# Optimization experiments

Measured on AMD Instinct MI355X. Metric: run time of the kernel, lower is better.

## Reference

```python
import jax, jax.numpy as jnp
import numpy as np

LAMBDA_SOFTMAX = 10.0  # opt.lambda_softmax
LEAKY_SLOPE = 0.1


def l2norm(x, axis):
    # matches torch F.normalize(p=2, eps=1e-12)
    n = jnp.linalg.norm(x, axis=axis, keepdims=True)
    return x / jnp.clip(n, 1e-12)


def setup_inputs() -> dict:
    key = jax.random.key(0)
    k1, k2, k3, k4, k5 = jax.random.split(key, 5)
    I, Q, T, S, D = 64, 49, 64, 64, 256  # n_img, n_region, n_txt, max_words, feature_size
    return {
        "local_img_query": jax.random.normal(k1, (I, Q, D), jnp.float32),
        "local_img_value": jax.random.normal(k2, (I, Q, D), jnp.float32),
        "local_text_key": jax.random.normal(k3, (T, S, D), jnp.float32),
        "local_text_value": jax.random.normal(k4, (T, S, D), jnp.float32),
        "text_length": jax.random.randint(k5, (T,), 8, S + 1, jnp.int32),
    }


def reference(local_img_query, local_img_value, local_text_key, local_text_value, text_length):
    # Vectorized form of the per-sentence Python loop in compute_i2t_sim.
    # Variable sentence lengths are handled with a mask over the padded word axis,
    # which reproduces the ragged torch math exactly (see comments).
    T, S, D = local_text_key.shape
    I, Q, _ = local_img_query.shape

    qn = l2norm(local_img_query, -1)   # [I,Q,D]
    kn = l2norm(local_text_key, -1)    # [T,S,D]

    # bmm(txt_key_norm, queryT): (B,S,D)x(B,D,Q) -> here [T,I,S,Q]
    attn = jnp.einsum('tsd,iqd->tisq', kn, qn)
    attn = jnp.where(attn > 0, attn, LEAKY_SLOPE * attn)      # LeakyReLU(0.1)
    # l2norm(attn, 2) normalizes over queryL per (t,i,s) row -> independent of padding
    attn = l2norm(attn, -1)
    attn = jnp.swapaxes(attn, 2, 3)                            # [T,I,Q,S]

    mask = jnp.arange(S)[None, :] < text_length[:, None]       # [T,S]
    logits = jnp.where(mask[:, None, None, :], attn * LAMBDA_SOFTMAX, -jnp.inf)
    attn = jax.nn.softmax(logits, axis=-1)                     # padded words -> exactly 0

    # focal_equal with sourceL = actual n_word of each sentence
    n_word = text_length.astype(attn.dtype)[:, None, None, None]
    funcF = attn * n_word - jnp.sum(attn, axis=-1, keepdims=True)
    fattn = (funcF > 0).astype(attn.dtype)                     # padded attn=0 -> funcF<0 -> 0
    tmp = fattn * attn
    attn = tmp / jnp.sum(tmp, axis=-1, keepdims=True)

    # bmm(valueT, attnT) -> weighted text context per (txt, img): [T,I,Q,D]
    wei = jnp.einsum('tsd,tiqs->tiqd', local_text_value, attn)
    wei = l2norm(wei, -1)

    # cosine similarity with image values along d, then mean over regions
    v = local_img_value[None]                                  # [1,I,Q,D]
    w12 = jnp.sum(v * wei, -1)
    denom = jnp.linalg.norm(v, axis=-1) * jnp.linalg.norm(wei, axis=-1)
    sim = w12 / jnp.clip(denom, 1e-8)                          # [T,I,Q]
    i2t = sim.mean(axis=-1)                                    # [T,I]
    return i2t.T                                               # [n_img, n_txt]
```

## Files before the change

### kernel.cpp

```cpp
#include <hip/hip_runtime.h>
#include <math.h>

#define I_N 64
#define Q_N 49
#define T_N 64
#define S_N 64
#define D_N 256

typedef __attribute__((ext_vector_type(8))) short short8;
typedef __attribute__((ext_vector_type(4))) float f32x4;
typedef unsigned short ushort_t;

__device__ __forceinline__ float waveReduceSum64(float v) {
    v += __shfl_xor(v, 1);
    v += __shfl_xor(v, 2);
    v += __shfl_xor(v, 4);
    v += __shfl_xor(v, 8);
    v += __shfl_xor(v, 16);
    v += __shfl_xor(v, 32);
    return v;
}

__device__ __forceinline__ ushort_t f2bf(float x) {
    unsigned u = __builtin_bit_cast(unsigned, x);
    unsigned r = (u + 0x7fffu + ((u >> 16) & 1u)) >> 16;
    return (ushort_t)r;
}
__device__ __forceinline__ float bf2f(ushort_t h) {
    unsigned u = ((unsigned)h) << 16;
    return __builtin_bit_cast(float, u);
}
__device__ __forceinline__ void split_bf16(float x, ushort_t& h, ushort_t& l) {
    h = f2bf(x);
    l = f2bf(x - bf2f(h));
}

__global__ void prep_all(const float* __restrict__ q_in, const float* __restrict__ v_in,
                         const float* __restrict__ k_in, const float* __restrict__ tv,
                         ushort_t* __restrict__ qfh, ushort_t* __restrict__ qfl,
                         ushort_t* __restrict__ kfh, ushort_t* __restrict__ kfl,
                         ushort_t* __restrict__ vfh, ushort_t* __restrict__ vfl,
                         float* __restrict__ vP, float* __restrict__ vnorm) {
    __shared__ float tile[64][65];
    __shared__ float ws[8];
    int b = blockIdx.x;
    int tid = threadIdx.x;

    if (b < 8192) {
        int isimg = (b < 4096) ? 1 : 0;
        int row = isimg ? b : (b - 4096);
        int hi = row >> 6, lo = row & 63;
        float x = 0.0f, vv = 0.0f;
        if (isimg) {
            if (lo < Q_N) {
                size_t base = ((size_t)hi * Q_N + lo) * D_N + tid;
                x = q_in[base];
                vv = v_in[base];
            }
        } else {
            x = k_in[(size_t)row * D_N + tid];
        }
        float s1 = waveReduceSum64(x * x);
        float s2 = waveReduceSum64(vv * vv);
        int wv = tid >> 6, ln = tid & 63;
        if (ln == 0) { ws[wv] = s1; ws[4 + wv] = s2; }
        __syncthreads();
        float n1 = sqrtf(ws[0] + ws[1] + ws[2] + ws[3]);
        float xn = x / fmaxf(n1, 1e-12f);
        ushort_t h, l;
        split_bf16(xn, h, l);
        size_t off = ((size_t)hi << 14) + (size_t)((((lo >> 4) * 8 + (tid >> 5))) << 9)
                   + (size_t)(((((tid >> 3) & 3) * 16 + (lo & 15))) << 3) + (tid & 7);
        if (isimg) {
            qfh[off] = h;
            qfl[off] = l;
            if (tid == 0) vnorm[row] = sqrtf(ws[4] + ws[5] + ws[6] + ws[7]);
        } else {
            kfh[off] = h;
            kfl[off] = l;
        }
    } else if (b < 8448) {
        int bb = b - 8192;
        int t = bb >> 2;
        int d0 = (bb & 3) * 64;
        const float* src = tv + ((size_t)t << 14) + d0;
        ushort_t* dh = vfh + ((size_t)t << 14);
        ushort_t* dl = vfl + ((size_t)t << 14);
#pragma unroll
        for (int r = 0; r < 16; ++r) {
            int idx = r * 256 + tid;
            int s = idx >> 6, d = idx & 63;
            tile[s][d] = src[s * D_N + d];
        }
        __syncthreads();
#pragma unroll
        for (int r = 0; r < 16; ++r) {
            int idx = r * 256 + tid;
            int d = idx >> 6, s = idx & 63;
            int dg = d0 + d;
            float x = tile[s][d];
            ushort_t h, l;
            split_bf16(x, h, l);
            int dgrp = dg >> 4, lrd = dg & 15;
            int k0g = s >> 5, lk3 = (s >> 3) & 3, e = s & 7;
            size_t off = (size_t)(dgrp << 10) + (k0g << 9) + ((lk3 * 16 + lrd) << 3) + e;
            dh[off] = h;
            dl[off] = l;
        }
    } else {
        int bb = b - 8448;
        int i = bb >> 3;
        int sub = bb & 7;
        const float* src = v_in + (size_t)i * Q_N * D_N;
        float* dst = vP + ((size_t)i << 14);
#pragma unroll
        for (int r2 = 0; r2 < 8; ++r2) {
            int rep = sub * 8 + r2;
            int o = rep * 256 + tid;
            int r = o & 3;
            int md = (o >> 2) & 3;
            int nq = (o >> 4) & 3;
            int lane = (o >> 6) & 63;
            int w = o >> 12;
            int lr = lane & 15, lk = lane >> 4;
            int q = nq * 16 + lr;
            int d = w * 64 + md * 16 + lk * 4 + r;
            dst[o] = (q < Q_N) ? src[q * D_N + d] : 0.0f;
        }
    }
}

__launch_bounds__(256, 4)
__global__ void i2t_mfma(const ushort_t* __restrict__ kfh, const ushort_t* __restrict__ kfl,
                         const ushort_t* __restrict__ qfh, const ushort_t* __restrict__ qfl,
                         const ushort_t* __restrict__ vfh, const ushort_t* __restrict__ vfl,
                         const float* __restrict__ vP,
                         const float* __restrict__ vnorm,
                         const int* __restrict__ tlen,
                         float* __restrict__ out)
{
    __shared__ __align__(16) unsigned char RK[33280];

    const int bid = blockIdx.x;
    const int xcd = bid & 7;
    const int j = bid >> 3;
    const int t = (xcd << 3) | (j & 7);
    const int i = j >> 3;

    const int tid = threadIdx.x;
    const int lane = tid & 63;
    const int w = tid >> 6;
    const int lr = lane & 15;
    const int lk = lane >> 4;

    const int wsr = (w >> 1) * 32;
    const int wq  = (w & 1) * 32;
    f32x4 acc[2][2];
#pragma unroll
    for (int a = 0; a < 2; ++a)
#pragma unroll
        for (int b2 = 0; b2 < 2; ++b2) acc[a][b2] = (f32x4){0.f, 0.f, 0.f, 0.f};
    {
        const ushort_t* kH = kfh + ((size_t)t << 14) + (size_t)(w >> 1) * 8192;
        const ushort_t* kL = kfl + ((size_t)t << 14) + (size_t)(w >> 1) * 8192;
        const ushort_t* qH = qfh + ((size_t)i << 14) + (size_t)(w & 1) * 8192;
        const ushort_t* qL = qfl + ((size_t)i << 14) + (size_t)(w & 1) * 8192;
#pragma unroll
        for (int k8 = 0; k8 < 8; ++k8) {
            int fo = k8 * 512 + lane * 8;
            short8 aH0 = *(const short8*)(kH + fo);
            short8 aL0 = *(const short8*)(kL + fo);
            short8 aH1 = *(const short8*)(kH + 4096 + fo);
            short8 aL1 = *(const short8*)(kL + 4096 + fo);
            short8 bH0 = *(const short8*)(qH + fo);
            short8 bL0 = *(const short8*)(qL + fo);
            short8 bH1 = *(const short8*)(qH + 4096 + fo);
            short8 bL1 = *(const short8*)(qL + 4096 + fo);
            acc[0][0] = __builtin_amdgcn_mfma_f32_16x16x32_bf16(aH0, bH0, acc[0][0], 0, 0, 0);
            acc[0][1] = __builtin_amdgcn_mfma_f32_16x16x32_bf16(aH0, bH1, acc[0][1], 0, 0, 0);
            acc[1][0] = __builtin_amdgcn_mfma_f32_16x16x32_bf16(aH1, bH0, acc[1][0], 0, 0, 0);
            acc[1][1] = __builtin_amdgcn_mfma_f32_16x16x32_bf16(aH1, bH1, acc[1][1], 0, 0, 0);
            acc[0][0] = __builtin_amdgcn_mfma_f32_16x16x32_bf16(aH0, bL0, acc[0][0], 0, 0, 0);
            acc[0][1] = __builtin_amdgcn_mfma_f32_16x16x32_bf16(aH0, bL1, acc[0][1], 0, 0, 0);
            acc[1][0] = __builtin_amdgcn_mfma_f32_16x16x32_bf16(aH1, bL0, acc[1][0], 0, 0, 0);
            acc[1][1] = __builtin_amdgcn_mfma_f32_16x16x32_bf16(aH1, bL1, acc[1][1], 0, 0, 0);
            acc[0][0] = __builtin_amdgcn_mfma_f32_16x16x32_bf16(aL0, bH0, acc[0][0], 0, 0, 0);
            acc[0][1] = __builtin_amdgcn_mfma_f32_16x16x32_bf16(aL0, bH1, acc[0][1], 0, 0, 0);
            acc[1][0] = __builtin_amdgcn_mfma_f32_16x16x32_bf16(aL1, bH0, acc[1][0], 0, 0, 0);
            acc[1][1] = __builtin_amdgcn_mfma_f32_16x16x32_bf16(aL1, bH1, acc[1][1], 0, 0, 0);
        }
    }
    {
        float* As = (float*)RK;
#pragma unroll
        for (int si = 0; si < 2; ++si)
#pragma unroll
            for (int qi = 0; qi < 2; ++qi)
#pragma unroll
                for (int r = 0; r < 4; ++r) {
                    int s = wsr + si * 16 + lk * 4 + r;
                    int q = wq + qi * 16 + lr;
                    float v = acc[si][qi][r];
                    v = (v > 0.0f) ? v : 0.1f * v;
                    As[s * 65 + q] = v;
                }
    }
    __syncthreads();

    {
        const float* As = (const float*)RK;
        float* rinv = (float*)(RK + 16640);
        int s = tid >> 2, part = tid & 3;
        float ss = 0.0f;
#pragma unroll
        for (int q0 = 0; q0 < 64; q0 += 4) {
            float v = As[s * 65 + q0 + part];
            ss += v * v;
        }
        ss += __shfl_xor(ss, 1);
        ss += __shfl_xor(ss, 2);
        if (part == 0) rinv[s] = 1.0f / fmaxf(sqrtf(ss), 1e-12f);
    }
    __syncthreads();

    const int len = tlen[t];
    {
        const float* As = (const float*)RK;
        const float* rinv = (const float*)(RK + 16640);
        ushort_t* Ph = (ushort_t*)(RK + 16896);
        ushort_t* Pl = (ushort_t*)(RK + 25088);
        const float thr = 1.0f / (float)len;
        int q = tid >> 2, part = tid & 3;
        float logit[16];
        float m = -INFINITY;
#pragma unroll
        for (int k = 0; k < 16; ++k) {
            int s = part * 16 + k;
            float lg = (s < len) ? 10.0f * As[s * 65 + q] * rinv[s] : -INFINITY;
            logit[k] = lg;
            m = fmaxf(m, lg);
        }
        m = fmaxf(m, __shfl_xor(m, 1));
        m = fmaxf(m, __shfl_xor(m, 2));
        float p[16];
        float sum = 0.0f;
#pragma unroll
        for (int k = 0; k < 16; ++k) {
            int s = part * 16 + k;
            float e = (s < len) ? __expf(logit[k] - m) : 0.0f;
            p[k] = e;
            sum += e;
        }
        sum += __shfl_xor(sum, 1);
        sum += __shfl_xor(sum, 2);
        float inv = 1.0f / sum;
        float sk = 0.0f;
#pragma unroll
        for (int k = 0; k < 16; ++k) {
            p[k] *= inv;
            if (p[k] > thr) sk += p[k];
        }
        sk += __shfl_xor(sk, 1);
        sk += __shfl_xor(sk, 2);
        float iv2 = 1.0f / sk;

        ushort_t hh[16], ll[16];
#pragma unroll
        for (int k = 0; k < 16; ++k) {
            float pv = (p[k] > thr) ? p[k] * iv2 : 0.0f;
            if (q >= Q_N) pv = 0.0f;
            split_bf16(pv, hh[k], ll[k]);
        }
        int c0 = (2 * part) ^ (q & 7);
        int c1 = (2 * part + 1) ^ (q & 7);
        short8 v0, v1;
#pragma unroll
        for (int k = 0; k < 8; ++k) { v0[k] = (short)hh[k]; v1[k] = (short)hh[k + 8]; }
        *(short8*)(Ph + q * 64 + (c0 << 3)) = v0;
        *(short8*)(Ph + q * 64 + (c1 << 3)) = v1;
#pragma unroll
        for (int k = 0; k < 8; ++k) { v0[k] = (short)ll[k]; v1[k] = (short)ll[k + 8]; }
        *(short8*)(Pl + q * 64 + (c0 << 3)) = v0;
        *(short8*)(Pl + q * 64 + (c1 << 3)) = v1;
    }
    __syncthreads();

    f32x4 acc2[4][4];
#pragma unroll
    for (int a = 0; a < 4; ++a)
#pragma unroll
        for (int b2 = 0; b2 < 4; ++b2) acc2[a][b2] = (f32x4){0.f, 0.f, 0.f, 0.f};
    {
        const ushort_t* vH = vfh + ((size_t)t << 14) + (size_t)w * 4096;
        const ushort_t* vL = vfl + ((size_t)t << 14) + (size_t)w * 4096;
        const ushort_t* PH = (const ushort_t*)(RK + 16896);
        const ushort_t* PL = (const ushort_t*)(RK + 25088);
#pragma unroll
        for (int k0g = 0; k0g < 2; ++k0g) {
#pragma unroll
            for (int md = 0; md < 4; ++md) {
                int vo = md * 1024 + k0g * 512 + lane * 8;
                short8 vh = *(const short8*)(vH + vo);
                short8 vl = *(const short8*)(vL + vo);
#pragma unroll
                for (int nq = 0; nq < 4; ++nq) {
                    int qrow = nq * 16 + lr;
                    int o = qrow * 64 + (((k0g * 4 + lk) ^ (qrow & 7)) << 3);
                    short8 ph = *(const short8*)(PH + o);
                    short8 pl = *(const short8*)(PL + o);
                    acc2[md][nq] = __builtin_amdgcn_mfma_f32_16x16x32_bf16(vh, ph, acc2[md][nq], 0, 0, 0);
                    acc2[md][nq] = __builtin_amdgcn_mfma_f32_16x16x32_bf16(vl, ph, acc2[md][nq], 0, 0, 0);
                    acc2[md][nq] = __builtin_amdgcn_mfma_f32_16x16x32_bf16(vh, pl, acc2[md][nq], 0, 0, 0);
                }
            }
        }
    }

    {
        float* wsq = (float*)RK;
        float* wdv = (float*)(RK + 1024);
        const float* vPb = vP + ((((size_t)i * 4 + w) * 64 + lane) << 6);
#pragma unroll
        for (int nq = 0; nq < 4; ++nq) {
            float s2 = 0.0f, dv = 0.0f;
#pragma unroll
            for (int md = 0; md < 4; ++md) {
                f32x4 vv = *(const f32x4*)(vPb + nq * 16 + md * 4);
#pragma unroll
                for (int r = 0; r < 4; ++r) {
                    float wv = acc2[md][nq][r];
                    s2 += wv * wv;
                    dv += wv * vv[r];
                }
            }
            s2 += __shfl_xor(s2, 16);
            s2 += __shfl_xor(s2, 32);
            dv += __shfl_xor(dv, 16);
            dv += __shfl_xor(dv, 32);
            if (lane < 16) {
                wsq[w * 64 + nq * 16 + lane] = s2;
                wdv[w * 64 + nq * 16 + lane] = dv;
            }
        }
    }
    __syncthreads();
    if (tid < 64) {
        const float* wsq = (const float*)RK;
        const float* wdv = (const float*)(RK + 1024);
        int q = tid;
        float s2 = 0.0f, dv = 0.0f;
#pragma unroll
        for (int ww = 0; ww < 4; ++ww) {
            s2 += wsq[ww * 64 + q];
            dv += wdv[ww * 64 + q];
        }
        float sim = 0.0f;
        if (q < Q_N) {
            float wn = sqrtf(s2);
            float w12 = dv / fmaxf(wn, 1e-12f);
            float wnn = wn / fmaxf(wn, 1e-12f);
            float denom = fmaxf(vnorm[i * 64 + q] * wnn, 1e-8f);
            sim = w12 / denom;
        }
        sim = waveReduceSum64(sim);
        if (tid == 0) out[(size_t)i * T_N + t] = sim * (1.0f / (float)Q_N);
    }
}

extern "C" void kernel_launch(void* const* d_in, const int* in_sizes, int n_in,
                              void* d_out, int out_size, void* d_ws, size_t ws_size,
                              hipStream_t stream) {
    const float* img_query = (const float*)d_in[0];
    const float* img_value = (const float*)d_in[1];
    const float* text_key  = (const float*)d_in[2];
    const float* text_val  = (const float*)d_in[3];
    const int*   text_len  = (const int*)d_in[4];
    float* out = (float*)d_out;

    const size_t NPAD = (size_t)64 * 64 * 256;
    ushort_t* qfh = (ushort_t*)d_ws;
    ushort_t* qfl = qfh + NPAD;
    ushort_t* kfh = qfl + NPAD;
    ushort_t* kfl = kfh + NPAD;
    ushort_t* vfh = kfl + NPAD;
    ushort_t* vfl = vfh + NPAD;
    float* vnorm  = (float*)(vfl + NPAD);
    float* vP     = vnorm + I_N * 64;

    prep_all<<<8960, 256, 0, stream>>>(img_query, img_value, text_key, text_val,
                                       qfh, qfl, kfh, kfl, vfh, vfl, vP, vnorm);

    i2t_mfma<<<T_N * I_N, 256, 0, stream>>>(kfh, kfl, qfh, qfl, vfh, vfl,
                                            vP, vnorm, text_len, out);
}
```

Measured before the change: 104.2 us.

## Compute row-norm and softmax in MFMA registers instead of staging through LDS

The first GEMM's accumulator tile is no longer written to a padded LDS matrix and re-read by a thread-per-query layout. LeakyReLU, row L2 norm, masked softmax and the focal threshold sums are now done directly on the accumulator fragments, using cross-lane shuffles plus small LDS exchanges between wave pairs. The softmax max subtraction is dropped, which relies on logits being bounded by ±10 after normalization. Shared memory shrinks from about 33 KB to about 20 KB, which may allow more resident blocks, at the cost of a few extra barriers.

```diff
diff --git a/kernel.cpp b/kernel.cpp
--- a/kernel.cpp
+++ b/kernel.cpp
@@ -8,6 +8,7 @@
 #define D_N 256
 
 typedef __attribute__((ext_vector_type(8))) short short8;
+typedef __attribute__((ext_vector_type(4))) short s16x4;
 typedef __attribute__((ext_vector_type(4))) float f32x4;
 typedef unsigned short ushort_t;
 
@@ -139,7 +140,7 @@
                          const int* __restrict__ tlen,
                          float* __restrict__ out)
 {
-    __shared__ __align__(16) unsigned char RK[33280];
+    __shared__ __align__(16) unsigned char RK[19968];
 
     const int bid = blockIdx.x;
     const int xcd = bid & 7;
@@ -190,98 +191,137 @@
             acc[1][1] = __builtin_amdgcn_mfma_f32_16x16x32_bf16(aL1, bH1, acc[1][1], 0, 0, 0);
         }
     }
-    {
-        float* As = (float*)RK;
+
+#pragma unroll
+    for (int si = 0; si < 2; ++si)
+#pragma unroll
+        for (int qi = 0; qi < 2; ++qi)
+#pragma unroll
+            for (int r = 0; r < 4; ++r) {
+                float v = acc[si][qi][r];
+                acc[si][qi][r] = (v > 0.0f) ? v : 0.1f * v;
+            }
+
+    {
+        float* rowp = (float*)(RK + 16384);
+        float ssv[2][4];
 #pragma unroll
         for (int si = 0; si < 2; ++si)
 #pragma unroll
-            for (int qi = 0; qi < 2; ++qi)
+            for (int r = 0; r < 4; ++r) {
+                float v0 = acc[si][0][r], v1 = acc[si][1][r];
+                float ss = v0 * v0 + v1 * v1;
+                ss += __shfl_xor(ss, 1);
+                ss += __shfl_xor(ss, 2);
+                ss += __shfl_xor(ss, 4);
+                ss += __shfl_xor(ss, 8);
+                ssv[si][r] = ss;
+            }
+        if (lr == 0) {
+#pragma unroll
+            for (int si = 0; si < 2; ++si)
+#pragma unroll
+                for (int r = 0; r < 4; ++r)
+                    rowp[w * 32 + si * 16 + lk * 4 + r] = ssv[si][r];
+        }
+        __syncthreads();
+        const float* prp = (const float*)(RK + 16384) + (w ^ 1) * 32;
+#pragma unroll
+        for (int si = 0; si < 2; ++si)
+#pragma unroll
+            for (int r = 0; r < 4; ++r) {
+                float tot = ssv[si][r] + prp[si * 16 + lk * 4 + r];
+                float rv = 10.0f / fmaxf(sqrtf(tot), 1e-12f);
+                acc[si][0][r] *= rv;
+                acc[si][1][r] *= rv;
+            }
+    }
+
+    const int len = tlen[t];
+    const float thr = 1.0f / (float)len;
+    float csum[2];
+    {
+        float* colp = (float*)(RK + 16896);
+#pragma unroll
+        for (int qi = 0; qi < 2; ++qi) {
+            float cs = 0.0f;
+#pragma unroll
+            for (int si = 0; si < 2; ++si)
 #pragma unroll
                 for (int r = 0; r < 4; ++r) {
                     int s = wsr + si * 16 + lk * 4 + r;
-                    int q = wq + qi * 16 + lr;
-                    float v = acc[si][qi][r];
-                    v = (v > 0.0f) ? v : 0.1f * v;
-                    As[s * 65 + q] = v;
+                    float e = (s < len) ? __expf(acc[si][qi][r]) : 0.0f;
+                    acc[si][qi][r] = e;
+                    cs += e;
                 }
-    }
-    __syncthreads();
-
-    {
-        const float* As = (const float*)RK;
-        float* rinv = (float*)(RK + 16640);
-        int s = tid >> 2, part = tid & 3;
-        float ss = 0.0f;
-#pragma unroll
-        for (int q0 = 0; q0 < 64; q0 += 4) {
-            float v = As[s * 65 + q0 + part];
-            ss += v * v;
-        }
-        ss += __shfl_xor(ss, 1);
-        ss += __shfl_xor(ss, 2);
-        if (part == 0) rinv[s] = 1.0f / fmaxf(sqrtf(ss), 1e-12f);
-    }
-    __syncthreads();
-
-    const int len = tlen[t];
-    {
-        const float* As = (const float*)RK;
-        const float* rinv = (const float*)(RK + 16640);
-        ushort_t* Ph = (ushort_t*)(RK + 16896);
-        ushort_t* Pl = (ushort_t*)(RK + 25088);
-        const float thr = 1.0f / (float)len;
-        int q = tid >> 2, part = tid & 3;
-        float logit[16];
-        float m = -INFINITY;
-#pragma unroll
-        for (int k = 0; k < 16; ++k) {
-            int s = part * 16 + k;
-            float lg = (s < len) ? 10.0f * As[s * 65 + q] * rinv[s] : -INFINITY;
-            logit[k] = lg;
-            m = fmaxf(m, lg);
-        }
-        m = fmaxf(m, __shfl_xor(m, 1));
-        m = fmaxf(m, __shfl_xor(m, 2));
-        float p[16];
-        float sum = 0.0f;
-#pragma unroll
-        for (int k = 0; k < 16; ++k) {
-            int s = part * 16 + k;
-            float e = (s < len) ? __expf(logit[k] - m) : 0.0f;
-            p[k] = e;
-            sum += e;
-        }
-        sum += __shfl_xor(sum, 1);
-        sum += __shfl_xor(sum, 2);
-        float inv = 1.0f / sum;
-        float sk = 0.0f;
-#pragma unroll
-        for (int k = 0; k < 16; ++k) {
-            p[k] *= inv;
-            if (p[k] > thr) sk += p[k];
-        }
-        sk += __shfl_xor(sk, 1);
-        sk += __shfl_xor(sk, 2);
-        float iv2 = 1.0f / sk;
-
-        ushort_t hh[16], ll[16];
-#pragma unroll
-        for (int k = 0; k < 16; ++k) {
-            float pv = (p[k] > thr) ? p[k] * iv2 : 0.0f;
-            if (q >= Q_N) pv = 0.0f;
-            split_bf16(pv, hh[k], ll[k]);
-        }
-        int c0 = (2 * part) ^ (q & 7);
-        int c1 = (2 * part + 1) ^ (q & 7);
-        short8 v0, v1;
-#pragma unroll
-        for (int k = 0; k < 8; ++k) { v0[k] = (short)hh[k]; v1[k] = (short)hh[k + 8]; }
-        *(short8*)(Ph + q * 64 + (c0 << 3)) = v0;
-        *(short8*)(Ph + q * 64 + (c1 << 3)) = v1;
-#pragma unroll
-        for (int k = 0; k < 8; ++k) { v0[k] = (short)ll[k]; v1[k] = (short)ll[k + 8]; }
-        *(short8*)(Pl + q * 64 + (c0 << 3)) = v0;
-        *(short8*)(Pl + q * 64 + (c1 << 3)) = v1;
+            cs += __shfl_xor(cs, 16);
+            cs += __shfl_xor(cs, 32);
+            csum[qi] = cs;
+        }
+        if (lk == 0) {
+            colp[w * 32 + lr] = csum[0];
+            colp[w * 32 + 16 + lr] = csum[1];
+        }
+        __syncthreads();
+        const float* pcp = (const float*)(RK + 16896) + (w ^ 2) * 32;
+        csum[0] += pcp[lr];
+        csum[1] += pcp[16 + lr];
+    }
+    float skv[2];
+    {
+        float* colp2 = (float*)(RK + 16896) + 128;
+#pragma unroll
+        for (int qi = 0; qi < 2; ++qi) {
+            float inv = 1.0f / csum[qi];
+            float sk = 0.0f;
+#pragma unroll
+            for (int si = 0; si < 2; ++si)
+#pragma unroll
+                for (int r = 0; r < 4; ++r) {
+                    float p = acc[si][qi][r] * inv;
+                    acc[si][qi][r] = p;
+                    if (p > thr) sk += p;
+                }
+            sk += __shfl_xor(sk, 16);
+            sk += __shfl_xor(sk, 32);
+            skv[qi] = sk;
+        }
+        if (lk == 0) {
+            colp2[w * 32 + lr] = skv[0];
+            colp2[w * 32 + 16 + lr] = skv[1];
+        }
+        __syncthreads();
+        const float* pk = (const float*)(RK + 16896) + 128 + (w ^ 2) * 32;
+        skv[0] += pk[lr];
+        skv[1] += pk[16 + lr];
+    }
+
+    {
+        ushort_t* Ph = (ushort_t*)RK;
+        ushort_t* Pl = (ushort_t*)(RK + 8192);
+#pragma unroll
+        for (int si = 0; si < 2; ++si)
+#pragma unroll
+            for (int qi = 0; qi < 2; ++qi) {
+                int q = wq + qi * 16 + lr;
+                float iv2 = 1.0f / skv[qi];
+                s16x4 vh, vl;
+#pragma unroll
+                for (int r = 0; r < 4; ++r) {
+                    float p = acc[si][qi][r];
+                    float pv = (p > thr) ? p * iv2 : 0.0f;
+                    if (q >= Q_N) pv = 0.0f;
+                    ushort_t hh, ll;
+                    split_bf16(pv, hh, ll);
+                    vh[r] = (short)hh;
+                    vl[r] = (short)ll;
+                }
+                int s0 = wsr + si * 16 + lk * 4;
+                int cidx = s0 >> 3;
+                int off = q * 64 + ((cidx ^ (q & 7)) << 3) + (s0 & 7);
+                *(s16x4*)(Ph + off) = vh;
+                *(s16x4*)(Pl + off) = vl;
+            }
     }
     __syncthreads();
 
@@ -293,8 +333,8 @@
     {
         const ushort_t* vH = vfh + ((size_t)t << 14) + (size_t)w * 4096;
         const ushort_t* vL = vfl + ((size_t)t << 14) + (size_t)w * 4096;
-        const ushort_t* PH = (const ushort_t*)(RK + 16896);
-        const ushort_t* PL = (const ushort_t*)(RK + 25088);
+        const ushort_t* PH = (const ushort_t*)RK;
+        const ushort_t* PL = (const ushort_t*)(RK + 8192);
 #pragma unroll
         for (int k0g = 0; k0g < 2; ++k0g) {
 #pragma unroll
@@ -317,8 +357,8 @@
     }
 
     {
-        float* wsq = (float*)RK;
-        float* wdv = (float*)(RK + 1024);
+        float* wsq = (float*)(RK + 17920);
+        float* wdv = (float*)(RK + 18944);
         const float* vPb = vP + ((((size_t)i * 4 + w) * 64 + lane) << 6);
 #pragma unroll
         for (int nq = 0; nq < 4; ++nq) {
@@ -345,8 +385,8 @@
     }
     __syncthreads();
     if (tid < 64) {
-        const float* wsq = (const float*)RK;
-        const float* wdv = (const float*)(RK + 1024);
+        const float* wsq = (const float*)(RK + 17920);
+        const float* wdv = (const float*)(RK + 18944);
         int q = tid;
         float s2 = 0.0f, dv = 0.0f;
 #pragma unroll
```

Measured after the change: 109.6 us. +5.3%, slower.
